# Performance work log

Measured on AMD Instinct MI355X. Metric: run time of the kernel, lower is better.

Reference implementation:

```python
import jax, jax.numpy as jnp
import numpy as np
from jax import lax

MAX_SIGMA = 20.0
TRUNCATE = 4.0  # scipy.ndimage.gaussian_filter default
R = int(TRUNCATE * MAX_SIGMA + 0.5)  # fixed max radius = 80 -> 161 taps


def setup_inputs() -> dict:
    key = jax.random.key(0)
    k1, k2 = jax.random.split(key)
    x = jax.random.normal(k1, (512, 256, 256), dtype=jnp.float32)
    blur_sigmas = jnp.geomspace(0.5, MAX_SIGMA, 32).astype(jnp.float32)
    fwd_steps = jax.random.randint(k2, (512,), 0, 32)
    return {"x": x, "blur_sigmas": blur_sigmas, "fwd_steps": fwd_steps}


def _per_sample_kernels(sigmas):
    # scipy gaussian_filter: radius_i = int(truncate*sigma + 0.5), kernel
    # phi(o) = exp(-o^2 / (2 sigma^2)) normalized over |o| <= radius_i.
    off = jnp.arange(-R, R + 1, dtype=jnp.float32)          # [2R+1]
    w = jnp.exp(-0.5 * (off[None, :] / sigmas[:, None]) ** 2)  # [B, 2R+1]
    rad = jnp.floor(TRUNCATE * sigmas + 0.5)[:, None]        # per-sample radius
    w = w * (jnp.abs(off)[None, :] <= rad)
    return w / jnp.sum(w, axis=-1, keepdims=True)


def _blur(x, kernels):
    # x: [B, H, W]; kernels: [B, 2R+1]. Separable depthwise conv, batch as
    # channels with feature_group_count=B; symmetric pad == scipy 'reflect'.
    B = x.shape[0]
    dn = ("NCHW", "OIHW", "NCHW")
    xp = jnp.pad(x, ((0, 0), (R, R), (R, R)), mode="symmetric")[None]  # [1,B,H+2R,W+2R]
    kh = kernels[:, None, :, None]  # [B,1,2R+1,1]
    kw = kernels[:, None, None, :]  # [B,1,1,2R+1]
    y = lax.conv_general_dilated(xp, kh, (1, 1), "VALID",
                                 dimension_numbers=dn, feature_group_count=B)
    y = lax.conv_general_dilated(y, kw, (1, 1), "VALID",
                                 dimension_numbers=dn, feature_group_count=B)
    return y[0]  # [B, H, W]


def reference(x, blur_sigmas, fwd_steps):
    sigmas = blur_sigmas[fwd_steps]           # [B] per-sample sigma
    kernels = _per_sample_kernels(sigmas)     # [B, 2R+1]
    return _blur(x, kernels)
```

## Files before the change

kernel.cpp:

```cpp
#include <hip/hip_runtime.h>

#define WDIM  256
#define NSAMP 512
#define NSIG  32
#define RB    32
#define NBAND 4096
#define QOFF  16
#define WOFF  65536

typedef float    f32x4 __attribute__((ext_vector_type(4)));
typedef _Float16 f16x8 __attribute__((ext_vector_type(8)));
typedef __fp16   fp16x2 __attribute__((ext_vector_type(2)));

__device__ __forceinline__ int reflect(int q) {
    q = (q < 0) ? (-q - 1) : q;
    return (q >= WDIM) ? (2 * WDIM - 1 - q) : q;
}

__global__ __launch_bounds__(256) void build_all(const float* __restrict__ sigmas,
                                                 const int* __restrict__ steps,
                                                 _Float16* __restrict__ Wg,
                                                 int* __restrict__ q) {
    int t = threadIdx.x;
    if (blockIdx.x < 256) {
        __shared__ float wl[161];
        __shared__ float red;
        int s = blockIdx.x >> 3, og = blockIdx.x & 7;
        float sigma = sigmas[s];
        float radf = floorf(4.0f * sigma + 0.5f);
        if (t < 161) {
            float off = (float)(t - 80);
            float w = 0.0f;
            if (fabsf(off) <= radf) { float z = off / sigma; w = expf(-0.5f * z * z); }
            wl[t] = w;
        }
        __syncthreads();
        if (t < 64) {
            float v = wl[t] + wl[t + 64] + (t < 33 ? wl[t + 128] : 0.0f);
            #pragma unroll
            for (int o = 32; o > 0; o >>= 1) v += __shfl_down(v, o);
            if (t == 0) red = 1.0f / v;
        }
        __syncthreads();
        float rs = red;
        int i = t;
        _Float16* wrow = Wg + ((size_t)s << 16) + (i << 8);
        for (int rq = og * 4; rq < og * 4 + 4; ++rq) {
            f16x8 v;
            #pragma unroll
            for (int j = 0; j < 8; ++j) {
                int r = rq * 8 + j;
                int d1 = r - i, d2 = -r - 1 - i, d3 = 511 - r - i;
                float w = 0.0f;
                if (d1 >= -80 && d1 <= 80) w += wl[d1 + 80];
                if (d2 >= -80)             w += wl[d2 + 80];
                if (d3 <= 80)              w += wl[d3 + 80];
                v[j] = (_Float16)(w * rs);
            }
            *(f16x8*)(wrow + rq * 8) = v;
        }
    } else {
        __shared__ int hist[32];
        __shared__ int base[32];
        if (t < 32) hist[t] = 0;
        __syncthreads();
        int nb2[2], rd2[2], st2[2];
        #pragma unroll
        for (int k = 0; k < 2; ++k) {
            int samp = t + 256 * k;
            int st = steps[samp];
            float sigma = sigmas[st];
            int rad = (int)floorf(4.0f * sigma + 0.5f);
            st2[k] = st; rd2[k] = rad;
            nb2[k] = (2 * rad + 15) >> 3;
            atomicAdd(&hist[nb2[k]], 1);
        }
        __syncthreads();
        if (t == 0) {
            int acc = 0;
            for (int bin = 31; bin >= 0; --bin) { base[bin] = acc; acc += hist[bin]; }
        }
        __syncthreads();
        #pragma unroll
        for (int k = 0; k < 2; ++k) {
            int samp = t + 256 * k;
            int r = atomicAdd(&base[nb2[k]], 1);
            int x = r & 7;
            int p = r >> 3;
            #pragma unroll
            for (int jb = 0; jb < 8; ++jb)
                q[QOFF + (((p << 3) + jb) << 3) + x] =
                    samp | (jb << 9) | (st2[k] << 12) | (rd2[k] << 17);
        }
    }
}

template <bool QUEUED>
__global__ __launch_bounds__(256, 2) void blur_mfma(const float* __restrict__ in,
                                                    float* __restrict__ out,
                                                    const float* __restrict__ sigmas,
                                                    const int* __restrict__ steps,
                                                    const int* __restrict__ q,
                                                    const _Float16* __restrict__ Wg) {
    __shared__ alignas(16) _Float16 YL[RB * WDIM];

    int b, r0, s, rad;
    if constexpr (QUEUED) {
        int d = q[QOFF + blockIdx.x];
        b   = d & 511;
        r0  = ((d >> 9) & 7) << 5;
        s   = (d >> 12) & 31;
        rad = (d >> 17) & 127;
    } else {
        int bid = blockIdx.x;
        int e = (bid & 7) * (NBAND / 8) + (bid >> 3);
        b = e >> 3; r0 = (e & 7) << 5;
        s = steps[b];
        rad = (int)floorf(4.0f * sigmas[s] + 0.5f);
    }
    const _Float16* Wm = Wg + ((size_t)s << 16);
    const float*    Xb = in + ((size_t)b << 16);

    int ln = threadIdx.x & 63, wv = threadIdx.x >> 6;
    int lm = ln & 15, lq = ln >> 4;

    f32x4 acc[2][4];
    #pragma unroll
    for (int mt = 0; mt < 2; ++mt)
        #pragma unroll
        for (int nt = 0; nt < 4; ++nt) acc[mt][nt] = (f32x4)0.0f;

    int kt0 = max(0, r0 - rad) >> 5;
    int kt1 = min(WDIM - 1, r0 + RB - 1 + rad) >> 5;

    float xvc[4][8], xvn[4][8];
    auto xload = [&](int kt, float (&dst)[4][8]) {
        const float* xp = Xb + (size_t)((kt << 5) + lq * 8) * WDIM + wv * 64 + lm;
        #pragma unroll
        for (int nt = 0; nt < 4; ++nt)
            #pragma unroll
            for (int jj = 0; jj < 8; ++jj)
                dst[nt][jj] = xp[(size_t)jj * WDIM + nt * 16];
    };
    auto vtile = [&](int kt, float (&xv)[4][8]) {
        f16x8 af[2];
        #pragma unroll
        for (int mt = 0; mt < 2; ++mt)
            af[mt] = *(const f16x8*)(Wm + (size_t)(r0 + mt * 16 + lm) * WDIM + (kt << 5) + lq * 8);
        #pragma unroll
        for (int nt = 0; nt < 4; ++nt) {
            union { f16x8 v; fp16x2 h[4]; } u;
            #pragma unroll
            for (int p = 0; p < 4; ++p)
                u.h[p] = __builtin_amdgcn_cvt_pkrtz(xv[nt][2 * p], xv[nt][2 * p + 1]);
            #pragma unroll
            for (int mt = 0; mt < 2; ++mt)
                acc[mt][nt] = __builtin_amdgcn_mfma_f32_16x16x32_f16(af[mt], u.v, acc[mt][nt], 0, 0, 0);
        }
    };

    xload(kt0, xvc);
    for (int kt = kt0; kt <= kt1; ++kt) {
        if (kt < kt1) xload(kt + 1, xvn);
        vtile(kt, xvc);
        if (kt < kt1) {
            #pragma unroll
            for (int nt = 0; nt < 4; ++nt)
                #pragma unroll
                for (int jj = 0; jj < 8; ++jj) xvc[nt][jj] = xvn[nt][jj];
        }
    }

    #pragma unroll
    for (int mt = 0; mt < 2; ++mt)
        #pragma unroll
        for (int nt = 0; nt < 4; ++nt)
            #pragma unroll
            for (int g = 0; g < 4; ++g) {
                int i = mt * 16 + lq * 4 + g;
                int c = wv * 64 + nt * 16 + lm;
                YL[(i << 8) + (c ^ ((i & 7) << 3))] = (_Float16)acc[mt][nt][g];
            }

    int jlo = wv * 64;
    int hk0 = max(0, jlo - rad) >> 5;
    int hk1 = min(WDIM - 1, jlo + 63 + rad) >> 5;

    f16x8 bfc[4], bfn[4];
    auto wload = [&](int kt, f16x8 (&bf)[4]) {
        #pragma unroll
        for (int nt = 0; nt < 4; ++nt)
            bf[nt] = *(const f16x8*)(Wm + (size_t)(jlo + nt * 16 + lm) * WDIM + (kt << 5) + lq * 8);
    };
    wload(hk0, bfc);
    __syncthreads();

    f32x4 hac[2][4];
    #pragma unroll
    for (int mt = 0; mt < 2; ++mt)
        #pragma unroll
        for (int nt = 0; nt < 4; ++nt) hac[mt][nt] = (f32x4)0.0f;

    for (int kt = hk0; kt <= hk1; ++kt) {
        if (kt < hk1) wload(kt + 1, bfn);
        f16x8 af[2];
        #pragma unroll
        for (int mt = 0; mt < 2; ++mt) {
            int i = mt * 16 + lm;
            int c0 = (kt << 5) + lq * 8;
            af[mt] = *(const f16x8*)&YL[(i << 8) + (c0 ^ ((i & 7) << 3))];
        }
        #pragma unroll
        for (int mt = 0; mt < 2; ++mt)
            #pragma unroll
            for (int nt = 0; nt < 4; ++nt)
                hac[mt][nt] = __builtin_amdgcn_mfma_f32_16x16x32_f16(af[mt], bfc[nt], hac[mt][nt], 0, 0, 0);
        if (kt < hk1) {
            #pragma unroll
            for (int nt = 0; nt < 4; ++nt) bfc[nt] = bfn[nt];
        }
    }

    float* ob = out + ((size_t)b << 16);
    #pragma unroll
    for (int mt = 0; mt < 2; ++mt)
        #pragma unroll
        for (int nt = 0; nt < 4; ++nt)
            #pragma unroll
            for (int g = 0; g < 4; ++g)
                ob[(size_t)(r0 + mt * 16 + lq * 4 + g) * WDIM + jlo + nt * 16 + lm] = hac[mt][nt][g];
}

__device__ __forceinline__ int make_weights161(int b, const float* __restrict__ sigmas,
                                               const int* __restrict__ steps,
                                               float* wl, float* red) {
    int t = threadIdx.x;
    float sigma = sigmas[steps[b]];
    float radf = floorf(4.0f * sigma + 0.5f);
    if (t < 192) {
        float w = 0.0f;
        if (t < 161) {
            float off = (float)(t - 80);
            if (fabsf(off) <= radf) { float z = off / sigma; w = expf(-0.5f * z * z); }
        }
        wl[t] = w;
    }
    __syncthreads();
    if (t < 64) {
        float v = wl[t] + wl[t + 64] + wl[t + 128];
        #pragma unroll
        for (int o = 32; o > 0; o >>= 1) v += __shfl_down(v, o);
        if (t == 0) red[0] = 1.0f / v;
    }
    __syncthreads();
    float rs = red[0];
    if (t < 161) wl[t] *= rs;
    __syncthreads();
    return (int)radf;
}

__global__ __launch_bounds__(256) void vblur_nt(const float* __restrict__ in,
                                                float* __restrict__ out,
                                                const float* __restrict__ sigmas,
                                                const int* __restrict__ steps) {
    __shared__ float wl[192];
    __shared__ float red[1];
    int bid = blockIdx.x;
    int b = bid >> 4, i0 = (bid & 15) * 16;
    int rad = make_weights161(b, sigmas, steps, wl, red);
    int j = threadIdx.x;
    const float* inb = in + (size_t)b * WDIM * WDIM;
    float acc[16];
    #pragma unroll
    for (int ii = 0; ii < 16; ++ii) acc[ii] = 0.0f;
    for (int u = -rad; u <= rad; ++u) {
        float w = wl[80 + u];
        #pragma unroll
        for (int ii = 0; ii < 16; ++ii)
            acc[ii] = fmaf(w, inb[reflect(i0 + ii + u) * WDIM + j], acc[ii]);
    }
    #pragma unroll
    for (int ii = 0; ii < 16; ++ii)
        out[((size_t)b * WDIM + (i0 + ii)) * WDIM + j] = acc[ii];
}

__global__ __launch_bounds__(256) void hblur_inplace(float* __restrict__ buf,
                                                     const float* __restrict__ sigmas,
                                                     const int* __restrict__ steps) {
    __shared__ float wl[192];
    __shared__ float red[1];
    __shared__ float rp[WDIM + 160];
    int bid = blockIdx.x;
    int b = bid >> 8, i = bid & 255;
    float* row = buf + ((size_t)b * WDIM + i) * WDIM;
    int t = threadIdx.x;
    for (int s = t; s < WDIM + 160; s += 256) rp[s] = row[reflect(s - 80)];
    int rad = make_weights161(b, sigmas, steps, wl, red);
    float acc = 0.0f;
    for (int u = -rad; u <= rad; ++u) acc = fmaf(wl[80 + u], rp[80 + t + u], acc);
    row[t] = acc;
}

extern "C" void kernel_launch(void* const* d_in, const int* in_sizes, int n_in,
                              void* d_out, int out_size, void* d_ws, size_t ws_size,
                              hipStream_t stream) {
    const float* x     = (const float*)d_in[0];
    const float* sig   = (const float*)d_in[1];
    const int*   steps = (const int*)d_in[2];
    float* out = (float*)d_out;

    const size_t need = (size_t)WOFF + (size_t)NSIG * WDIM * WDIM * 2;
    if (ws_size >= need) {
        int* q = (int*)d_ws;
        _Float16* Wg = (_Float16*)((char*)d_ws + WOFF);
        build_all<<<257, 256, 0, stream>>>(sig, steps, Wg, q);
        blur_mfma<true><<<NBAND, 256, 0, stream>>>(x, out, sig, steps, q, Wg);
    } else {
        vblur_nt<<<NSAMP * 16, 256, 0, stream>>>(x, out, sig, steps);
        hblur_inplace<<<NSAMP * WDIM, 256, 0, stream>>>(out, sig, steps);
    }
}
```

Baseline: 86.39 us.

## Unroll blur tile loops with ping-pong buffers and raise occupancy to three blocks

The vertical and horizontal MFMA tile loops are fully unrolled up to a fixed maximum tile count, using alternating A/B register buffers. This removes the per-iteration register copies of prefetched data. The weight fragments for the vertical pass and the first horizontal weight tile are now prefetched early, overlapping with earlier work. Launch bounds move from 2 to 3 blocks per SM for more latency hiding, at the cost of tighter register budgets and possible spills, since two activation buffers and extra fragments are live at once.

```diff
diff --git a/kernel.cpp b/kernel.cpp
--- a/kernel.cpp
+++ b/kernel.cpp
@@ -7,6 +7,7 @@
 #define NBAND 4096
 #define QOFF  16
 #define WOFF  65536
+#define MAXT  7
 
 typedef float    f32x4 __attribute__((ext_vector_type(4)));
 typedef _Float16 f16x8 __attribute__((ext_vector_type(8)));
@@ -96,7 +97,7 @@
 }
 
 template <bool QUEUED>
-__global__ __launch_bounds__(256, 2) void blur_mfma(const float* __restrict__ in,
+__global__ __launch_bounds__(256, 3) void blur_mfma(const float* __restrict__ in,
                                                     float* __restrict__ out,
                                                     const float* __restrict__ sigmas,
                                                     const int* __restrict__ steps,
@@ -124,16 +125,23 @@
     int ln = threadIdx.x & 63, wv = threadIdx.x >> 6;
     int lm = ln & 15, lq = ln >> 4;
 
-    f32x4 acc[2][4];
-    #pragma unroll
-    for (int mt = 0; mt < 2; ++mt)
-        #pragma unroll
-        for (int nt = 0; nt < 4; ++nt) acc[mt][nt] = (f32x4)0.0f;
-
     int kt0 = max(0, r0 - rad) >> 5;
     int kt1 = min(WDIM - 1, r0 + RB - 1 + rad) >> 5;
-
-    float xvc[4][8], xvn[4][8];
+    int ktn = kt1 - kt0;
+    int jlo = wv * 64;
+    int hk0 = max(0, jlo - rad) >> 5;
+    int hk1 = min(WDIM - 1, jlo + 63 + rad) >> 5;
+    int htn = hk1 - hk0;
+
+    f32x4 acc[2][4];
+    #pragma unroll
+    for (int mt = 0; mt < 2; ++mt)
+        #pragma unroll
+        for (int nt = 0; nt < 4; ++nt) acc[mt][nt] = (f32x4)0.0f;
+
+    float xva[4][8], xvb[4][8];
+    f16x8 afa[2], afb[2], bfa[4], bfb[4];
+
     auto xload = [&](int kt, float (&dst)[4][8]) {
         const float* xp = Xb + (size_t)((kt << 5) + lq * 8) * WDIM + wv * 64 + lm;
         #pragma unroll
@@ -142,11 +150,17 @@
             for (int jj = 0; jj < 8; ++jj)
                 dst[nt][jj] = xp[(size_t)jj * WDIM + nt * 16];
     };
-    auto vtile = [&](int kt, float (&xv)[4][8]) {
-        f16x8 af[2];
+    auto afload = [&](int kt, f16x8 (&af)[2]) {
         #pragma unroll
         for (int mt = 0; mt < 2; ++mt)
             af[mt] = *(const f16x8*)(Wm + (size_t)(r0 + mt * 16 + lm) * WDIM + (kt << 5) + lq * 8);
+    };
+    auto wload = [&](int kt, f16x8 (&bf)[4]) {
+        #pragma unroll
+        for (int nt = 0; nt < 4; ++nt)
+            bf[nt] = *(const f16x8*)(Wm + (size_t)(jlo + nt * 16 + lm) * WDIM + (kt << 5) + lq * 8);
+    };
+    auto vtile = [&](f16x8 (&af)[2], float (&xv)[4][8]) {
         #pragma unroll
         for (int nt = 0; nt < 4; ++nt) {
             union { f16x8 v; fp16x2 h[4]; } u;
@@ -159,15 +173,20 @@
         }
     };
 
-    xload(kt0, xvc);
-    for (int kt = kt0; kt <= kt1; ++kt) {
-        if (kt < kt1) xload(kt + 1, xvn);
-        vtile(kt, xvc);
-        if (kt < kt1) {
-            #pragma unroll
-            for (int nt = 0; nt < 4; ++nt)
-                #pragma unroll
-                for (int jj = 0; jj < 8; ++jj) xvc[nt][jj] = xvn[nt][jj];
+    afload(kt0, afa);
+    xload(kt0, xva);
+    wload(hk0, bfa);
+
+    #pragma unroll
+    for (int kti = 0; kti < MAXT; ++kti) {
+        if (kti > ktn) break;
+        int kt = kt0 + kti;
+        if ((kti & 1) == 0) {
+            if (kti < ktn) { afload(kt + 1, afb); xload(kt + 1, xvb); }
+            vtile(afa, xva);
+        } else {
+            if (kti < ktn) { afload(kt + 1, afa); xload(kt + 1, xva); }
+            vtile(afb, xvb);
         }
     }
 
@@ -181,18 +200,6 @@
                 int c = wv * 64 + nt * 16 + lm;
                 YL[(i << 8) + (c ^ ((i & 7) << 3))] = (_Float16)acc[mt][nt][g];
             }
-
-    int jlo = wv * 64;
-    int hk0 = max(0, jlo - rad) >> 5;
-    int hk1 = min(WDIM - 1, jlo + 63 + rad) >> 5;
-
-    f16x8 bfc[4], bfn[4];
-    auto wload = [&](int kt, f16x8 (&bf)[4]) {
-        #pragma unroll
-        for (int nt = 0; nt < 4; ++nt)
-            bf[nt] = *(const f16x8*)(Wm + (size_t)(jlo + nt * 16 + lm) * WDIM + (kt << 5) + lq * 8);
-    };
-    wload(hk0, bfc);
     __syncthreads();
 
     f32x4 hac[2][4];
@@ -201,8 +208,7 @@
         #pragma unroll
         for (int nt = 0; nt < 4; ++nt) hac[mt][nt] = (f32x4)0.0f;
 
-    for (int kt = hk0; kt <= hk1; ++kt) {
-        if (kt < hk1) wload(kt + 1, bfn);
+    auto htile = [&](int kt, f16x8 (&bf)[4]) {
         f16x8 af[2];
         #pragma unroll
         for (int mt = 0; mt < 2; ++mt) {
@@ -214,10 +220,19 @@
         for (int mt = 0; mt < 2; ++mt)
             #pragma unroll
             for (int nt = 0; nt < 4; ++nt)
-                hac[mt][nt] = __builtin_amdgcn_mfma_f32_16x16x32_f16(af[mt], bfc[nt], hac[mt][nt], 0, 0, 0);
-        if (kt < hk1) {
-            #pragma unroll
-            for (int nt = 0; nt < 4; ++nt) bfc[nt] = bfn[nt];
+                hac[mt][nt] = __builtin_amdgcn_mfma_f32_16x16x32_f16(af[mt], bf[nt], hac[mt][nt], 0, 0, 0);
+    };
+
+    #pragma unroll
+    for (int hti = 0; hti < MAXT; ++hti) {
+        if (hti > htn) break;
+        int kt = hk0 + hti;
+        if ((hti & 1) == 0) {
+            if (hti < htn) wload(kt + 1, bfb);
+            htile(kt, bfa);
+        } else {
+            if (hti < htn) wload(kt + 1, bfa);
+            htile(kt, bfb);
         }
     }
 
```

Measured after the change: 85.97 us. No clear change (-0.5%).
